# Optimization experiments

Hardware: AMD Instinct MI355X
Metric: run time of the kernel (lower is better)

Reference implementation:

```python
import jax, jax.numpy as jnp
import numpy as np

B, C, D = 4, 1024, 1024
H, DH = 16, 64  # num_heads, head_size; D == H*DH


def setup_inputs() -> dict:
    key = jax.random.key(0)
    ks = jax.random.split(key, 8)
    return {
        "query_input": jax.random.normal(ks[0], (B, C, D), dtype=jnp.float32),
        "key_input": jax.random.normal(ks[1], (B, C, D), dtype=jnp.float32),
        "value_input": jax.random.normal(ks[2], (B, C, D), dtype=jnp.float32),
        "Wq": jax.random.normal(ks[3], (D, D), dtype=jnp.float32) * 0.02,
        "Wk": jax.random.normal(ks[4], (D, D), dtype=jnp.float32) * 0.02,
        "Wv": jax.random.normal(ks[5], (D, D), dtype=jnp.float32) * 0.02,
        "Wp": jax.random.normal(ks[6], (D, D), dtype=jnp.float32) * 0.02,
        "bp": jax.random.normal(ks[7], (D,), dtype=jnp.float32) * 0.02,
        "mask": jnp.zeros((C, C), dtype=bool),
    }


def _split_heads(x):
    # (B, C, D) -> (B, H, C, DH)
    return x.reshape(B, C, H, DH).transpose(0, 2, 1, 3)


def reference(query_input, key_input, value_input, Wq, Wk, Wv, Wp, bp, mask):
    scale = DH ** -0.5
    q = _split_heads(query_input @ Wq.T)
    k = _split_heads(key_input @ Wk.T)
    v = _split_heads(value_input @ Wv.T)
    # ||q_i - k_j||_2 via norm decomposition: |q|^2 + |k|^2 - 2 q.k
    q2 = jnp.sum(q * q, axis=-1)  # (B, H, C)
    k2 = jnp.sum(k * k, axis=-1)  # (B, H, C)
    qk = jnp.einsum("bhqd,bhkd->bhqk", q, k)  # (B, H, C, C)
    sq = jnp.maximum(q2[..., :, None] + k2[..., None, :] - 2.0 * qk, 0.0)
    wei = jnp.sqrt(sq) * scale
    wei = jnp.where(mask, -jnp.inf, wei)
    wei = jax.nn.softmax(wei, axis=-1)
    out = jnp.einsum("bhqk,bhkd->bhqd", wei, v)  # (B, H, C, DH)
    out = out.transpose(0, 2, 1, 3).reshape(B, C, D)
    return out @ Wp.T + bp
```

## Files before the change

### kernel.cpp

```cpp
#include <hip/hip_runtime.h>


typedef _Float16 f16;
typedef __attribute__((ext_vector_type(2))) _Float16 f16x2;
typedef __attribute__((ext_vector_type(8))) _Float16 f16x8;
typedef __attribute__((ext_vector_type(4))) float f32x4;
typedef __attribute__((ext_vector_type(16))) float f32x16;

#define MFMA16(a, b, c) __builtin_amdgcn_mfma_f32_16x16x32_f16((a), (b), (c), 0, 0, 0)
#define MFMA32(a, b, c) __builtin_amdgcn_mfma_f32_32x32x16_f16((a), (b), (c), 0, 0, 0)

constexpr double LOG2E = 1.4426950408889634;
constexpr double C2d = 0.015625 * LOG2E * LOG2E;

#if __has_builtin(__builtin_amdgcn_exp2f)
#define EXP2F(x) __builtin_amdgcn_exp2f(x)
#else
#define EXP2F(x) exp2f(x)
#endif
#if __has_builtin(__builtin_amdgcn_sqrtf)
#define SQRTF(x) __builtin_amdgcn_sqrtf(x)
#else
#define SQRTF(x) sqrtf(x)
#endif

__device__ __forceinline__ void stage16(const void* g, void* lds_base_uniform) {
#if __has_builtin(__builtin_amdgcn_global_load_lds)
    __builtin_amdgcn_global_load_lds((const __attribute__((address_space(1))) void*)g,
                                     (__attribute__((address_space(3))) void*)lds_base_uniform,
                                     16, 0, 0);
#else
    const int lane = threadIdx.x & 63;
    *(f16x8*)((f16*)lds_base_uniform + lane * 8) = *(const f16x8*)g;
#endif
}

__device__ __forceinline__ f16x8 cvt8v(f32x4 a, f32x4 b) {
    f16x8 o;
    o[0] = (f16)a[0]; o[1] = (f16)a[1]; o[2] = (f16)a[2]; o[3] = (f16)a[3];
    o[4] = (f16)b[0]; o[5] = (f16)b[1]; o[6] = (f16)b[2]; o[7] = (f16)b[3];
    return o;
}

__global__ __launch_bounds__(256) void cvt_all(const float* __restrict__ Xq,
                                               const float* __restrict__ Xk,
                                               const float* __restrict__ Xv,
                                               const float* __restrict__ Wq,
                                               const float* __restrict__ Wk,
                                               const float* __restrict__ Wv,
                                               const float* __restrict__ Wp,
                                               f16* __restrict__ W16,
                                               f16* __restrict__ X16) {
    const size_t idx = (size_t)blockIdx.x * 2048 + threadIdx.x * 8;
    const size_t M4 = 4ull << 20, M1 = 1ull << 20;
    const float* s;
    f16* d;
    if (idx < 3 * M4) {
        if (idx < M4) s = Xq + idx;
        else if (idx < 2 * M4) s = Xk + (idx - M4);
        else s = Xv + (idx - 2 * M4);
        d = X16 + idx;
    } else {
        size_t wi = idx - 3 * M4;
        if (wi < M1) s = Wq + wi;
        else if (wi < 2 * M1) s = Wk + (wi - M1);
        else if (wi < 3 * M1) s = Wv + (wi - 2 * M1);
        else s = Wp + (wi - 3 * M1);
        d = W16 + wi;
    }
    f32x4 a = *(const f32x4*)s;
    f32x4 b = *(const f32x4*)(s + 4);
    *(f16x8*)d = cvt8v(a, b);
}

template <bool NORMS, bool F32OUT>
__device__ __forceinline__ void gemm128(f16* As, f16* Bs,
                                        const f16* __restrict__ Ap,
                                        const f16* __restrict__ Bp,
                                        f16* __restrict__ Cop,
                                        float* __restrict__ Cf,
                                        const float* __restrict__ bias,
                                        float* __restrict__ nrmp,
                                        float osc, float nscale,
                                        int row0, int col0, int N, int K) {
    const int tid = threadIdx.x;
    const int lane = tid & 63;
    const int w = tid >> 6;
    const int l31 = lane & 31, l5 = lane >> 5;
    const int wr = (w >> 1) * 64, wc = (w & 1) * 64;

    f32x16 acc[2][2] = {};

    for (int kt = 0; kt < K; kt += 64) {
        __syncthreads();
#pragma unroll
        for (int t = 0; t < 4; ++t) {
            const int rb = w * 32 + t * 8;
            const int rr = rb + (lane >> 3);
            const int gs = (lane & 7) ^ (rr & 7);
            stage16(&Ap[(size_t)(row0 + rr) * K + kt + gs * 8], &As[rb * 64]);
            stage16(&Bp[(size_t)(col0 + rr) * K + kt + gs * 8], &Bs[rb * 64]);
        }
        __syncthreads();
#pragma unroll
        for (int ks = 0; ks < 4; ++ks) {
            const int gq = ks * 2 + l5;
            f16x8 af[2], bf[2];
#pragma unroll
            for (int mr = 0; mr < 2; ++mr)
                af[mr] = *(const f16x8*)&As[(wr + mr * 32 + l31) * 64 + ((gq ^ (l31 & 7)) * 8)];
#pragma unroll
            for (int n2 = 0; n2 < 2; ++n2)
                bf[n2] = *(const f16x8*)&Bs[(wc + n2 * 32 + l31) * 64 + ((gq ^ (l31 & 7)) * 8)];
#pragma unroll
            for (int mr = 0; mr < 2; ++mr)
#pragma unroll
                for (int n2 = 0; n2 < 2; ++n2) acc[mr][n2] = MFMA32(af[mr], bf[n2], acc[mr][n2]);
        }
    }

    const int cc0 = col0 + wc + l31;
    const int cc1 = col0 + wc + 32 + l31;
    const int hh = (col0 + wc) >> 6;
#pragma unroll
    for (int mr = 0; mr < 2; ++mr)
#pragma unroll
        for (int j = 0; j < 16; ++j) {
            const int rr = row0 + wr + mr * 32 + (j & 3) + 8 * (j >> 2) + 4 * l5;
            if (F32OUT) {
                Cf[(size_t)rr * N + cc0] = acc[mr][0][j] + bias[cc0];
                Cf[(size_t)rr * N + cc1] = acc[mr][1][j] + bias[cc1];
            } else {
                const f16 h0 = (f16)(acc[mr][0][j] * osc);
                const f16 h1 = (f16)(acc[mr][1][j] * osc);
                if (NORMS) {
                    float v0 = (float)h0, v1 = (float)h1;
                    float s = v0 * v0 + v1 * v1;
                    s += __shfl_xor(s, 1);
                    s += __shfl_xor(s, 2);
                    s += __shfl_xor(s, 4);
                    s += __shfl_xor(s, 8);
                    s += __shfl_xor(s, 16);
                    if (l31 == 0)
                        nrmp[(size_t)((rr >> 10) * 16 + hh) * 1024 + (rr & 1023)] = s * nscale;
                }
                Cop[(size_t)rr * N + cc0] = h0;
                Cop[(size_t)rr * N + cc1] = h1;
            }
        }
}

__global__ __launch_bounds__(256, 2) void gemm_qkv(const f16* __restrict__ X16,
                                                   const f16* __restrict__ W16,
                                                   f16* __restrict__ qb_base,
                                                   f16* __restrict__ vTb,
                                                   float* __restrict__ nrm,
                                                   float qsc, float ns_q, float ns_k) {
    __shared__ __attribute__((aligned(16))) f16 As[128 * 64];
    __shared__ __attribute__((aligned(16))) f16 Bs[128 * 64];
    const int bid = blockIdx.x;
    if (bid < 512) {
        const int z = bid & 1;
        const int t = (((bid & 7) >> 1) << 6) | (bid >> 3);
        const int row0 = (t >> 3) * 128;
        const int col0 = (t & 7) * 128;
        gemm128<true, false>(As, Bs,
                             X16 + (size_t)z * (4u << 20), W16 + (size_t)z * (1u << 20),
                             qb_base + (size_t)z * (4u << 20), nullptr, nullptr,
                             nrm + (size_t)z * 65536,
                             z ? 1.0f : qsc, z ? ns_k : ns_q, row0, col0, 1024, 1024);
    } else {
        const int f2 = bid - 512;
        const int x = f2 & 7, j = f2 >> 3;
        const int col0 = (x * 4 + (j & 3)) * 128;
        const int row0 = (j >> 2) * 128;
        gemm128<false, false>(As, Bs,
                              W16 + 2 * (1u << 20), X16 + 2 * (4u << 20),
                              vTb, nullptr, nullptr, nullptr,
                              1.0f, 0.f, row0, col0, 4096, 1024);
    }
}

__global__ __launch_bounds__(256, 2) void gemm_fin(const f16* __restrict__ A,
                                                   const f16* __restrict__ B,
                                                   float* __restrict__ Cf,
                                                   const float* __restrict__ bias) {
    __shared__ __attribute__((aligned(16))) f16 As[64 * 64];
    __shared__ __attribute__((aligned(16))) f16 Bs[128 * 64];
    const int tid = threadIdx.x;
    const int lane = tid & 63;
    const int w = tid >> 6;
    const int l31 = lane & 31, l5 = lane >> 5;
    const int wr = (w & 1) * 32, wc = (w >> 1) * 64;
    const int f = blockIdx.x;
    const int g = (f & 7) * 64 + (f >> 3);
    const int row0 = (g >> 3) * 64, col0 = (g & 7) * 128;
    const int K = 1024, N = 1024;

    f32x16 acc[2] = {};

    for (int kt = 0; kt < K; kt += 64) {
        __syncthreads();
#pragma unroll
        for (int t = 0; t < 2; ++t) {
            const int rb = w * 16 + t * 8;
            const int rr = rb + (lane >> 3);
            const int gs = (lane & 7) ^ (rr & 7);
            stage16(&A[(size_t)(row0 + rr) * K + kt + gs * 8], &As[rb * 64]);
        }
#pragma unroll
        for (int t = 0; t < 4; ++t) {
            const int rb = w * 32 + t * 8;
            const int rr = rb + (lane >> 3);
            const int gs = (lane & 7) ^ (rr & 7);
            stage16(&B[(size_t)(col0 + rr) * K + kt + gs * 8], &Bs[rb * 64]);
        }
        __syncthreads();
#pragma unroll
        for (int ks = 0; ks < 4; ++ks) {
            const int gq = ks * 2 + l5;
            f16x8 af = *(const f16x8*)&As[(wr + l31) * 64 + ((gq ^ (l31 & 7)) * 8)];
#pragma unroll
            for (int n2 = 0; n2 < 2; ++n2) {
                f16x8 bf = *(const f16x8*)&Bs[(wc + n2 * 32 + l31) * 64 + ((gq ^ (l31 & 7)) * 8)];
                acc[n2] = MFMA32(af, bf, acc[n2]);
            }
        }
    }

    const int cc0 = col0 + wc + l31;
    const int cc1 = col0 + wc + 32 + l31;
#pragma unroll
    for (int j = 0; j < 16; ++j) {
        const int rr = row0 + wr + (j & 3) + 8 * (j >> 2) + 4 * l5;
        Cf[(size_t)rr * N + cc0] = acc[0][j] + bias[cc0];
        Cf[(size_t)rr * N + cc1] = acc[1][j] + bias[cc1];
    }
}

__global__ __launch_bounds__(256, 2) void attn(const f16* __restrict__ qs,
                                               const f16* __restrict__ kb,
                                               const f16* __restrict__ vT,
                                               const float* __restrict__ q2c2,
                                               const float* __restrict__ k2c2,
                                               f16* __restrict__ out) {
    __shared__ __attribute__((aligned(16))) f16 Ks[128 * 64];
    __shared__ __attribute__((aligned(16))) f16 Vs[64 * 128];
    __shared__ float k2tile[128];
    const int tid = threadIdx.x;
    const int lane = tid & 63;
    const int w = tid >> 6;
    const int l15 = lane & 15, l4 = lane >> 4;
    const int fid = blockIdx.y * 16 + blockIdx.x;
    const int qt = (fid >> 3) & 15;
    const int bh = (fid & 7) * 8 + (fid >> 7);
    const int b = bh >> 4, h = bh & 15;
    const int wq = w * 16;
    const int hcol = h * 64;
    const int qrow0 = b * 1024 + qt * 64;
    const f16* vTh = vT + (size_t)hcol * 4096 + b * 1024;

    const int sr = tid >> 3, sc0 = (tid & 7) * 8;
    const int vr = tid >> 4, vc0 = (tid & 15) * 8;
    const int vsw = (vr & 7) << 3;
    const int fsw = (l15 & 7) << 3;

    f16x8 bq[2];
#pragma unroll
    for (int ks = 0; ks < 2; ++ks)
        bq[ks] = *(const f16x8*)&qs[(size_t)(qrow0 + wq + l15) * 1024 + hcol + ks * 32 + l4 * 8];
    const float q2m = q2c2[(size_t)bh * 1024 + qt * 64 + wq + l15];

    f32x4 accv[4] = {};
    f32x4 dacc = {};
    const f16 one = (f16)1.f;
    const f16x8 ones8 = {one, one, one, one, one, one, one, one};

    f16x8 kreg[4], vreg[4];
    float k2reg = 0.f;
#define ISSUE_LOADS(KT)                                                                                      \
    {                                                                                                        \
        _Pragma("unroll") for (int i = 0; i < 4; ++i)                                                        \
            kreg[i] = *(const f16x8*)&kb[(size_t)(b * 1024 + (KT) * 128 + sr + i * 32) * 1024 + hcol + sc0]; \
        _Pragma("unroll") for (int j = 0; j < 4; ++j)                                                        \
            vreg[j] = *(const f16x8*)&vTh[(size_t)(vr + j * 16) * 4096 + (KT) * 128 + vc0];                  \
        k2reg = (tid < 128) ? k2c2[(size_t)bh * 1024 + (KT) * 128 + tid] : 0.f;                              \
    }

    ISSUE_LOADS(0)

    for (int kt = 0; kt < 8; ++kt) {
        __syncthreads();
#pragma unroll
        for (int i = 0; i < 4; ++i) {
            const int kap = sr + i * 32;
            const int s = ((kap >> 5) & 3) * 32 + ((kap >> 2) & 1) * 16 + ((kap >> 3) & 3) * 4 + (kap & 3);
            *(f16x8*)&Ks[s * 64 + (sc0 ^ ((s & 7) << 3))] = kreg[i];
        }
#pragma unroll
        for (int j = 0; j < 4; ++j) *(f16x8*)&Vs[(vr + j * 16) * 128 + (vc0 ^ vsw)] = vreg[j];
        if (tid < 128) k2tile[tid] = k2reg;
        __syncthreads();
        if (kt < 7) ISSUE_LOADS(kt + 1)

        f16x8 kfb[2][4];
#pragma unroll
        for (int hh = 0; hh < 2; ++hh) {
            kfb[0][hh * 2] = *(const f16x8*)&Ks[(hh * 16 + l15) * 64 + ((l4 * 8) ^ fsw)];
            kfb[0][hh * 2 + 1] = *(const f16x8*)&Ks[(hh * 16 + l15) * 64 + ((32 + l4 * 8) ^ fsw)];
        }
#pragma unroll
        for (int kk = 0; kk < 4; ++kk) {
            const int cb = kk & 1;
            if (kk < 3) {
#pragma unroll
                for (int hh = 0; hh < 2; ++hh) {
                    const int n_ = (kk + 1) * 2 + hh;
                    kfb[cb ^ 1][hh * 2] = *(const f16x8*)&Ks[(n_ * 16 + l15) * 64 + ((l4 * 8) ^ fsw)];
                    kfb[cb ^ 1][hh * 2 + 1] = *(const f16x8*)&Ks[(n_ * 16 + l15) * 64 + ((32 + l4 * 8) ^ fsw)];
                }
            }
            f16x8 vf[4];
#pragma unroll
            for (int n2 = 0; n2 < 4; ++n2)
                vf[n2] = *(const f16x8*)&Vs[(n2 * 16 + l15) * 128 + ((kk * 32 + l4 * 8) ^ fsw)];

            unsigned um[4];
#pragma unroll
            for (int half = 0; half < 2; ++half) {
                f32x4 k2q = *(const f32x4*)&k2tile[kk * 32 + l4 * 8 + half * 4];
                f32x4 c0;
#pragma unroll
                for (int r = 0; r < 4; ++r) c0[r] = q2m + k2q[r];
                f32x4 st = MFMA16(kfb[cb][half * 2], bq[0], c0);
                st = MFMA16(kfb[cb][half * 2 + 1], bq[1], st);
                float p0 = EXP2F(SQRTF(fmaxf(st[0], 0.f)));
                float p1 = EXP2F(SQRTF(fmaxf(st[1], 0.f)));
                float p2 = EXP2F(SQRTF(fmaxf(st[2], 0.f)));
                float p3 = EXP2F(SQRTF(fmaxf(st[3], 0.f)));
                f16x2 lo = {(f16)p0, (f16)p1};
                f16x2 hi = {(f16)p2, (f16)p3};
                um[half * 2] = __builtin_bit_cast(unsigned, lo);
                um[half * 2 + 1] = __builtin_bit_cast(unsigned, hi);
            }
            uint4 u = {um[0], um[1], um[2], um[3]};
            f16x8 ap = __builtin_bit_cast(f16x8, u);
            dacc = MFMA16(ap, ones8, dacc);
#pragma unroll
            for (int n2 = 0; n2 < 4; ++n2) accv[n2] = MFMA16(ap, vf[n2], accv[n2]);
        }
    }

#pragma unroll
    for (int r = 0; r < 4; ++r) {
        const float rd = 1.0f / dacc[r];
#pragma unroll
        for (int n2 = 0; n2 < 4; ++n2)
            out[(size_t)(qrow0 + wq + l4 * 4 + r) * 1024 + hcol + n2 * 16 + l15] =
                (f16)(accv[n2][r] * rd);
    }
}

extern "C" void kernel_launch(void* const* d_in, const int* in_sizes, int n_in,
                              void* d_out, int out_size, void* d_ws, size_t ws_size,
                              hipStream_t stream) {
    const float* Xq = (const float*)d_in[0];
    const float* Xk = (const float*)d_in[1];
    const float* Xv = (const float*)d_in[2];
    const float* Wq = (const float*)d_in[3];
    const float* Wk = (const float*)d_in[4];
    const float* Wv = (const float*)d_in[5];
    const float* Wp = (const float*)d_in[6];
    const float* bp = (const float*)d_in[7];
    float* out = (float*)d_out;

    char* ws = (char*)d_ws;
    f16* W16 = (f16*)(ws);
    f16* X16 = (f16*)(ws + (8ull << 20));
    f16* qb = (f16*)(ws + (32ull << 20));
    f16* kb = (f16*)(ws + (40ull << 20));
    f16* vTb = (f16*)(ws + (48ull << 20));
    f16* attnout = (f16*)(ws + (56ull << 20));
    (void)kb;
    float* q2c2 = out;
    float* k2c2 = out + 65536;

    const float qsc = (float)(-2.0 * C2d);
    const float ns_q = (float)(1.0 / (4.0 * C2d));
    const float ns_k = (float)C2d;

    cvt_all<<<8192, 256, 0, stream>>>(Xq, Xk, Xv, Wq, Wk, Wv, Wp, W16, X16);

    gemm_qkv<<<768, 256, 0, stream>>>(X16, W16, qb, vTb, q2c2, qsc, ns_q, ns_k);

    attn<<<dim3(16, 64), 256, 0, stream>>>(qb, kb, vTb, q2c2, k2c2, attnout);

    gemm_fin<<<512, 256, 0, stream>>>(attnout, W16 + 3 * (1u << 20), out, bp);
}
```

Baseline: 103.1 us.

## Double-buffer LDS tiles in GEMM and attention kernels to cut barriers

Switches the QKV GEMM, final projection GEMM and attention kernel to two shared-memory buffers that alternate per K step. The next tile is staged into the idle buffer while MFMAs read the current one, so each iteration needs one barrier instead of two. This doubles LDS use (64 KB per block in gemm_qkv), which may lower occupancy below the two blocks per CU the launch bounds target.

```diff
diff --git a/kernel.cpp b/kernel.cpp
--- a/kernel.cpp
+++ b/kernel.cpp
@@ -74,15 +74,15 @@
 }
 
 template <bool NORMS, bool F32OUT>
-__device__ __forceinline__ void gemm128(f16* As, f16* Bs,
-                                        const f16* __restrict__ Ap,
-                                        const f16* __restrict__ Bp,
-                                        f16* __restrict__ Cop,
-                                        float* __restrict__ Cf,
-                                        const float* __restrict__ bias,
-                                        float* __restrict__ nrmp,
-                                        float osc, float nscale,
-                                        int row0, int col0, int N, int K) {
+__device__ __forceinline__ void gemm128_db(f16 (*As)[128 * 64], f16 (*Bs)[128 * 64],
+                                           const f16* __restrict__ Ap,
+                                           const f16* __restrict__ Bp,
+                                           f16* __restrict__ Cop,
+                                           float* __restrict__ Cf,
+                                           const float* __restrict__ bias,
+                                           float* __restrict__ nrmp,
+                                           float osc, float nscale,
+                                           int row0, int col0, int N) {
     const int tid = threadIdx.x;
     const int lane = tid & 63;
     const int w = tid >> 6;
@@ -91,33 +91,38 @@
 
     f32x16 acc[2][2] = {};
 
-    for (int kt = 0; kt < K; kt += 64) {
-        __syncthreads();
-#pragma unroll
-        for (int t = 0; t < 4; ++t) {
-            const int rb = w * 32 + t * 8;
-            const int rr = rb + (lane >> 3);
-            const int gs = (lane & 7) ^ (rr & 7);
-            stage16(&Ap[(size_t)(row0 + rr) * K + kt + gs * 8], &As[rb * 64]);
-            stage16(&Bp[(size_t)(col0 + rr) * K + kt + gs * 8], &Bs[rb * 64]);
-        }
-        __syncthreads();
+#define STAGE_AB(KT, BUF)                                                                \
+    _Pragma("unroll") for (int t = 0; t < 4; ++t) {                                      \
+        const int rb = w * 32 + t * 8;                                                   \
+        const int rr = rb + (lane >> 3);                                                 \
+        const int gs = (lane & 7) ^ (rr & 7);                                            \
+        stage16(&Ap[(size_t)(row0 + rr) * 1024 + (KT) + gs * 8], &As[BUF][rb * 64]);     \
+        stage16(&Bp[(size_t)(col0 + rr) * 1024 + (KT) + gs * 8], &Bs[BUF][rb * 64]);     \
+    }
+
+    STAGE_AB(0, 0)
+    __syncthreads();
+    for (int it = 0; it < 16; ++it) {
+        const int cur = it & 1;
+        if (it < 15) STAGE_AB((it + 1) * 64, cur ^ 1)
 #pragma unroll
         for (int ks = 0; ks < 4; ++ks) {
             const int gq = ks * 2 + l5;
             f16x8 af[2], bf[2];
 #pragma unroll
             for (int mr = 0; mr < 2; ++mr)
-                af[mr] = *(const f16x8*)&As[(wr + mr * 32 + l31) * 64 + ((gq ^ (l31 & 7)) * 8)];
+                af[mr] = *(const f16x8*)&As[cur][(wr + mr * 32 + l31) * 64 + ((gq ^ (l31 & 7)) * 8)];
 #pragma unroll
             for (int n2 = 0; n2 < 2; ++n2)
-                bf[n2] = *(const f16x8*)&Bs[(wc + n2 * 32 + l31) * 64 + ((gq ^ (l31 & 7)) * 8)];
+                bf[n2] = *(const f16x8*)&Bs[cur][(wc + n2 * 32 + l31) * 64 + ((gq ^ (l31 & 7)) * 8)];
 #pragma unroll
             for (int mr = 0; mr < 2; ++mr)
 #pragma unroll
                 for (int n2 = 0; n2 < 2; ++n2) acc[mr][n2] = MFMA32(af[mr], bf[n2], acc[mr][n2]);
         }
-    }
+        __syncthreads();
+    }
+#undef STAGE_AB
 
     const int cc0 = col0 + wc + l31;
     const int cc1 = col0 + wc + 32 + l31;
@@ -156,28 +161,28 @@
                                                    f16* __restrict__ vTb,
                                                    float* __restrict__ nrm,
                                                    float qsc, float ns_q, float ns_k) {
-    __shared__ __attribute__((aligned(16))) f16 As[128 * 64];
-    __shared__ __attribute__((aligned(16))) f16 Bs[128 * 64];
+    __shared__ __attribute__((aligned(16))) f16 As[2][128 * 64];
+    __shared__ __attribute__((aligned(16))) f16 Bs[2][128 * 64];
     const int bid = blockIdx.x;
     if (bid < 512) {
         const int z = bid & 1;
         const int t = (((bid & 7) >> 1) << 6) | (bid >> 3);
         const int row0 = (t >> 3) * 128;
         const int col0 = (t & 7) * 128;
-        gemm128<true, false>(As, Bs,
-                             X16 + (size_t)z * (4u << 20), W16 + (size_t)z * (1u << 20),
-                             qb_base + (size_t)z * (4u << 20), nullptr, nullptr,
-                             nrm + (size_t)z * 65536,
-                             z ? 1.0f : qsc, z ? ns_k : ns_q, row0, col0, 1024, 1024);
+        gemm128_db<true, false>(As, Bs,
+                                X16 + (size_t)z * (4u << 20), W16 + (size_t)z * (1u << 20),
+                                qb_base + (size_t)z * (4u << 20), nullptr, nullptr,
+                                nrm + (size_t)z * 65536,
+                                z ? 1.0f : qsc, z ? ns_k : ns_q, row0, col0, 1024);
     } else {
         const int f2 = bid - 512;
         const int x = f2 & 7, j = f2 >> 3;
         const int col0 = (x * 4 + (j & 3)) * 128;
         const int row0 = (j >> 2) * 128;
-        gemm128<false, false>(As, Bs,
-                              W16 + 2 * (1u << 20), X16 + 2 * (4u << 20),
-                              vTb, nullptr, nullptr, nullptr,
-                              1.0f, 0.f, row0, col0, 4096, 1024);
+        gemm128_db<false, false>(As, Bs,
+                                 W16 + 2 * (1u << 20), X16 + 2 * (4u << 20),
+                                 vTb, nullptr, nullptr, nullptr,
+                                 1.0f, 0.f, row0, col0, 4096);
     }
 }
 
@@ -185,8 +190,8 @@
                                                    const f16* __restrict__ B,
                                                    float* __restrict__ Cf,
                                                    const float* __restrict__ bias) {
-    __shared__ __attribute__((aligned(16))) f16 As[64 * 64];
-    __shared__ __attribute__((aligned(16))) f16 Bs[128 * 64];
+    __shared__ __attribute__((aligned(16))) f16 As[2][64 * 64];
+    __shared__ __attribute__((aligned(16))) f16 Bs[2][128 * 64];
     const int tid = threadIdx.x;
     const int lane = tid & 63;
     const int w = tid >> 6;
@@ -195,38 +200,42 @@
     const int f = blockIdx.x;
     const int g = (f & 7) * 64 + (f >> 3);
     const int row0 = (g >> 3) * 64, col0 = (g & 7) * 128;
-    const int K = 1024, N = 1024;
+    const int N = 1024;
 
     f32x16 acc[2] = {};
 
-    for (int kt = 0; kt < K; kt += 64) {
-        __syncthreads();
-#pragma unroll
-        for (int t = 0; t < 2; ++t) {
-            const int rb = w * 16 + t * 8;
-            const int rr = rb + (lane >> 3);
-            const int gs = (lane & 7) ^ (rr & 7);
-            stage16(&A[(size_t)(row0 + rr) * K + kt + gs * 8], &As[rb * 64]);
-        }
-#pragma unroll
-        for (int t = 0; t < 4; ++t) {
-            const int rb = w * 32 + t * 8;
-            const int rr = rb + (lane >> 3);
-            const int gs = (lane & 7) ^ (rr & 7);
-            stage16(&B[(size_t)(col0 + rr) * K + kt + gs * 8], &Bs[rb * 64]);
-        }
-        __syncthreads();
+#define STAGE_FIN(KT, BUF)                                                               \
+    _Pragma("unroll") for (int t = 0; t < 2; ++t) {                                      \
+        const int rb = w * 16 + t * 8;                                                   \
+        const int rr = rb + (lane >> 3);                                                 \
+        const int gs = (lane & 7) ^ (rr & 7);                                            \
+        stage16(&A[(size_t)(row0 + rr) * 1024 + (KT) + gs * 8], &As[BUF][rb * 64]);      \
+    }                                                                                    \
+    _Pragma("unroll") for (int t = 0; t < 4; ++t) {                                      \
+        const int rb = w * 32 + t * 8;                                                   \
+        const int rr = rb + (lane >> 3);                                                 \
+        const int gs = (lane & 7) ^ (rr & 7);                                            \
+        stage16(&B[(size_t)(col0 + rr) * 1024 + (KT) + gs * 8], &Bs[BUF][rb * 64]);      \
+    }
+
+    STAGE_FIN(0, 0)
+    __syncthreads();
+    for (int it = 0; it < 16; ++it) {
+        const int cur = it & 1;
+        if (it < 15) STAGE_FIN((it + 1) * 64, cur ^ 1)
 #pragma unroll
         for (int ks = 0; ks < 4; ++ks) {
             const int gq = ks * 2 + l5;
-            f16x8 af = *(const f16x8*)&As[(wr + l31) * 64 + ((gq ^ (l31 & 7)) * 8)];
+            f16x8 af = *(const f16x8*)&As[cur][(wr + l31) * 64 + ((gq ^ (l31 & 7)) * 8)];
 #pragma unroll
             for (int n2 = 0; n2 < 2; ++n2) {
-                f16x8 bf = *(const f16x8*)&Bs[(wc + n2 * 32 + l31) * 64 + ((gq ^ (l31 & 7)) * 8)];
+                f16x8 bf = *(const f16x8*)&Bs[cur][(wc + n2 * 32 + l31) * 64 + ((gq ^ (l31 & 7)) * 8)];
                 acc[n2] = MFMA32(af, bf, acc[n2]);
             }
         }
-    }
+        __syncthreads();
+    }
+#undef STAGE_FIN
 
     const int cc0 = col0 + wc + l31;
     const int cc1 = col0 + wc + 32 + l31;
@@ -244,9 +253,9 @@
                                                const float* __restrict__ q2c2,
                                                const float* __restrict__ k2c2,
                                                f16* __restrict__ out) {
-    __shared__ __attribute__((aligned(16))) f16 Ks[128 * 64];
-    __shared__ __attribute__((aligned(16))) f16 Vs[64 * 128];
-    __shared__ float k2tile[128];
+    __shared__ __attribute__((aligned(16))) f16 Ks[2][128 * 64];
+    __shared__ __attribute__((aligned(16))) f16 Vs[2][64 * 128];
+    __shared__ float k2t[2][128];
     const int tid = threadIdx.x;
     const int lane = tid & 63;
     const int w = tid >> 6;
@@ -286,28 +295,31 @@
             vreg[j] = *(const f16x8*)&vTh[(size_t)(vr + j * 16) * 4096 + (KT) * 128 + vc0];                  \
         k2reg = (tid < 128) ? k2c2[(size_t)bh * 1024 + (KT) * 128 + tid] : 0.f;                              \
     }
+#define WRITE_TILE(BUF)                                                                                      \
+    {                                                                                                        \
+        _Pragma("unroll") for (int i = 0; i < 4; ++i) {                                                      \
+            const int kap = sr + i * 32;                                                                     \
+            const int s_ = ((kap >> 5) & 3) * 32 + ((kap >> 2) & 1) * 16 + ((kap >> 3) & 3) * 4 + (kap & 3); \
+            *(f16x8*)&Ks[BUF][s_ * 64 + (sc0 ^ ((s_ & 7) << 3))] = kreg[i];                                  \
+        }                                                                                                    \
+        _Pragma("unroll") for (int j = 0; j < 4; ++j)                                                        \
+            *(f16x8*)&Vs[BUF][(vr + j * 16) * 128 + (vc0 ^ vsw)] = vreg[j];                                  \
+        if (tid < 128) k2t[BUF][tid] = k2reg;                                                                \
+    }
 
     ISSUE_LOADS(0)
+    WRITE_TILE(0)
+    __syncthreads();
 
     for (int kt = 0; kt < 8; ++kt) {
-        __syncthreads();
-#pragma unroll
-        for (int i = 0; i < 4; ++i) {
-            const int kap = sr + i * 32;
-            const int s = ((kap >> 5) & 3) * 32 + ((kap >> 2) & 1) * 16 + ((kap >> 3) & 3) * 4 + (kap & 3);
-            *(f16x8*)&Ks[s * 64 + (sc0 ^ ((s & 7) << 3))] = kreg[i];
-        }
-#pragma unroll
-        for (int j = 0; j < 4; ++j) *(f16x8*)&Vs[(vr + j * 16) * 128 + (vc0 ^ vsw)] = vreg[j];
-        if (tid < 128) k2tile[tid] = k2reg;
-        __syncthreads();
+        const int cur = kt & 1;
         if (kt < 7) ISSUE_LOADS(kt + 1)
 
         f16x8 kfb[2][4];
 #pragma unroll
         for (int hh = 0; hh < 2; ++hh) {
-            kfb[0][hh * 2] = *(const f16x8*)&Ks[(hh * 16 + l15) * 64 + ((l4 * 8) ^ fsw)];
-            kfb[0][hh * 2 + 1] = *(const f16x8*)&Ks[(hh * 16 + l15) * 64 + ((32 + l4 * 8) ^ fsw)];
+            kfb[0][hh * 2] = *(const f16x8*)&Ks[cur][(hh * 16 + l15) * 64 + ((l4 * 8) ^ fsw)];
+            kfb[0][hh * 2 + 1] = *(const f16x8*)&Ks[cur][(hh * 16 + l15) * 64 + ((32 + l4 * 8) ^ fsw)];
         }
 #pragma unroll
         for (int kk = 0; kk < 4; ++kk) {
@@ -316,19 +328,19 @@
 #pragma unroll
                 for (int hh = 0; hh < 2; ++hh) {
                     const int n_ = (kk + 1) * 2 + hh;
-                    kfb[cb ^ 1][hh * 2] = *(const f16x8*)&Ks[(n_ * 16 + l15) * 64 + ((l4 * 8) ^ fsw)];
-                    kfb[cb ^ 1][hh * 2 + 1] = *(const f16x8*)&Ks[(n_ * 16 + l15) * 64 + ((32 + l4 * 8) ^ fsw)];
+                    kfb[cb ^ 1][hh * 2] = *(const f16x8*)&Ks[cur][(n_ * 16 + l15) * 64 + ((l4 * 8) ^ fsw)];
+                    kfb[cb ^ 1][hh * 2 + 1] = *(const f16x8*)&Ks[cur][(n_ * 16 + l15) * 64 + ((32 + l4 * 8) ^ fsw)];
                 }
             }
             f16x8 vf[4];
 #pragma unroll
             for (int n2 = 0; n2 < 4; ++n2)
-                vf[n2] = *(const f16x8*)&Vs[(n2 * 16 + l15) * 128 + ((kk * 32 + l4 * 8) ^ fsw)];
+                vf[n2] = *(const f16x8*)&Vs[cur][(n2 * 16 + l15) * 128 + ((kk * 32 + l4 * 8) ^ fsw)];
 
             unsigned um[4];
 #pragma unroll
             for (int half = 0; half < 2; ++half) {
-                f32x4 k2q = *(const f32x4*)&k2tile[kk * 32 + l4 * 8 + half * 4];
+                f32x4 k2q = *(const f32x4*)&k2t[cur][kk * 32 + l4 * 8 + half * 4];
                 f32x4 c0;
 #pragma unroll
                 for (int r = 0; r < 4; ++r) c0[r] = q2m + k2q[r];
@@ -349,7 +361,12 @@
 #pragma unroll
             for (int n2 = 0; n2 < 4; ++n2) accv[n2] = MFMA16(ap, vf[n2], accv[n2]);
         }
-    }
+
+        if (kt < 7) WRITE_TILE(cur ^ 1)
+        __syncthreads();
+    }
+#undef ISSUE_LOADS
+#undef WRITE_TILE
 
 #pragma unroll
     for (int r = 0; r < 4; ++r) {
```

New measurement: 120.0 us. 16.5% more time.
